# Optimization experiments

Measured on AMD Instinct MI355X. Metric: run time of the kernel, lower is better.

## Reference

```python
import jax, jax.numpy as jnp
import numpy as np

N_LOCS = 500_000
NUM_NEAREST = 100
L = 8192
K = 16


def setup_inputs() -> dict:
    key = jax.random.key(0)
    k1, k2, k3, k4 = jax.random.split(key, 4)
    # KNN index: for each location, its num_nearest neighbor location ids (1-indexed)
    nearby_locs = jax.random.randint(k1, (N_LOCS, NUM_NEAREST), 1, N_LOCS + 1, dtype=jnp.int32)
    # pop_freqs[i] = log(loc2freq[neighbor]+1); keep float for a differentiable analogue
    raw = jax.random.randint(k2, (N_LOCS, NUM_NEAREST), 1, 1000).astype(jnp.float32)
    pop_freqs = jnp.log(raw + 1.0)
    probs = pop_freqs / jnp.sum(pop_freqs, axis=1, keepdims=True)
    pop_cum_prob = jnp.cumsum(probs, axis=1)  # sorted ascending per row, ends ~1.0
    trg_seq = jax.random.randint(k3, (L, 2), 0, N_LOCS, dtype=jnp.int32)
    u = jax.random.uniform(k4, (L, K), dtype=jnp.float32)  # the random.random() draws
    return {
        "trg_seq": trg_seq,
        "k": K,
        "u": u,
        "nearby_locs": nearby_locs,
        "pop_freqs": pop_freqs,
        "pop_cum_prob": pop_cum_prob,
    }


def reference(trg_seq, k, u, nearby_locs, pop_freqs, pop_cum_prob):
    # rows: trg_loc - 1, clipped in-range (original indexes loc2freq with loc-1)
    rows = jnp.clip(trg_seq[:, 1] - 1, 0, N_LOCS - 1)          # [L]
    cum = pop_cum_prob[rows]                                   # [L, NUM_NEAREST] gather
    # bisect_left(row, u, hi=NUM_NEAREST-1) == min(searchsorted_left(row, u), NUM_NEAREST-1)
    idx = jax.vmap(lambda c, x: jnp.searchsorted(c, x, side="left"))(cum, u)  # [L, K]
    idx = jnp.minimum(idx, NUM_NEAREST - 1)
    neg_samples = jnp.take_along_axis(nearby_locs[rows], idx, axis=1).astype(jnp.int32)
    sample_probs = jnp.take_along_axis(pop_freqs[rows], idx, axis=1).astype(jnp.float32)
    return neg_samples, sample_probs
```

## Files before the change

### kernel.cpp

```cpp
#include <hip/hip_runtime.h>

#define N_LOCS_C 500000
#define NN 100
#define KK 16
#define LL 8192

__global__ __launch_bounds__(256)
void knn_pop_sampler_kernel(const int*   __restrict__ trg_seq,
                            const float* __restrict__ u,
                            const int*   __restrict__ nearby,
                            const float* __restrict__ freqs,
                            const float* __restrict__ cum,
                            float*       __restrict__ out_samples,
                            float*       __restrict__ out_probs)
{
    int t = blockIdx.x * blockDim.x + threadIdx.x;
    if (t >= LL * KK) return;

    int i = t >> 4;
    int loc = trg_seq[2 * i + 1] - 1;
    loc = min(max(loc, 0), N_LOCS_C - 1);

    float x = u[t];

    const float* crow = cum + (long long)loc * NN;
    int cnt = 0;
#pragma unroll
    for (int e = 0; e < NN; e += 4) {
        float4 v = *reinterpret_cast<const float4*>(crow + e);
        cnt += (v.x < x) + (v.y < x) + (v.z < x) + (v.w < x);
    }
    int idx = min(cnt, NN - 1);

    long long base = (long long)loc * NN + idx;
    out_samples[t] = (float)nearby[base];
    out_probs[t]   = freqs[base];
}

extern "C" void kernel_launch(void* const* d_in, const int* in_sizes, int n_in,
                              void* d_out, int out_size, void* d_ws, size_t ws_size,
                              hipStream_t stream) {
    const int*   trg_seq = (const int*)  d_in[0];
    const float* u       = (const float*)d_in[2];
    const int*   nearby  = (const int*)  d_in[3];
    const float* freqs   = (const float*)d_in[4];
    const float* cum     = (const float*)d_in[5];

    float* out = (float*)d_out;
    float* out_samples = out;
    float* out_probs   = out + LL * KK;

    const int total  = LL * KK;
    const int block  = 256;
    const int grid   = (total + block - 1) / block;
    knn_pop_sampler_kernel<<<grid, block, 0, stream>>>(
        trg_seq, u, nearby, freqs, cum, out_samples, out_probs);
}
```

Before: 9.710 us.

## Split each sample across two lanes and prefetch guessed gather row entry

```diff
diff --git a/kernel.cpp b/kernel.cpp
--- a/kernel.cpp
+++ b/kernel.cpp
@@ -14,27 +14,44 @@
                             float*       __restrict__ out_samples,
                             float*       __restrict__ out_probs)
 {
-    int t = blockIdx.x * blockDim.x + threadIdx.x;
-    if (t >= LL * KK) return;
+    int tt = blockIdx.x * blockDim.x + threadIdx.x;
+    int p  = tt >> 1;
+    int h  = tt & 1;
+    int i  = p >> 4;
 
-    int i = t >> 4;
     int loc = trg_seq[2 * i + 1] - 1;
     loc = min(max(loc, 0), N_LOCS_C - 1);
+    long long rowbase = (long long)loc * NN;
 
-    float x = u[t];
+    float x = u[p];
 
-    const float* crow = cum + (long long)loc * NN;
+    const float* gtab = h ? freqs : (const float*)(const void*)nearby;
+
+    int g = (int)(x * (float)NN);
+    g = min(max(g, 0), NN - 1);
+    float pf = gtab[rowbase + g];
+    asm volatile("" :: "v"(pf));
+
+    const float* crow = cum + rowbase;
+    int start = h * 52;
     int cnt = 0;
 #pragma unroll
-    for (int e = 0; e < NN; e += 4) {
-        float4 v = *reinterpret_cast<const float4*>(crow + e);
+    for (int q = 0; q < 48; q += 4) {
+        float4 v = *reinterpret_cast<const float4*>(crow + start + q);
         cnt += (v.x < x) + (v.y < x) + (v.z < x) + (v.w < x);
     }
+    {
+        float4 v = *reinterpret_cast<const float4*>(crow + 48);
+        int extra = (v.x < x) + (v.y < x) + (v.z < x) + (v.w < x);
+        cnt += h ? 0 : extra;
+    }
+    cnt += __shfl_xor(cnt, 1);
     int idx = min(cnt, NN - 1);
 
-    long long base = (long long)loc * NN + idx;
-    out_samples[t] = (float)nearby[base];
-    out_probs[t]   = freqs[base];
+    float raw = gtab[rowbase + idx];
+    float val = h ? raw : (float)__float_as_int(raw);
+    float* optr = h ? out_probs : out_samples;
+    optr[p] = val;
 }
 
 extern "C" void kernel_launch(void* const* d_in, const int* in_sizes, int n_in,
@@ -50,7 +67,7 @@
     float* out_samples = out;
     float* out_probs   = out + LL * KK;
 
-    const int total  = LL * KK;
+    const int total  = 2 * LL * KK;
     const int block  = 256;
     const int grid   = (total + block - 1) / block;
     knn_pop_sampler_kernel<<<grid, block, 0, stream>>>(
```

Result: no change. 9.746 us (+0.4%).
